# Kernel tuning notes

Measured on AMD Instinct MI355X. Metric: run time of the kernel, lower is better.

The kernel has to match this reference:

```python
import jax, jax.numpy as jnp
import numpy as np

B, N, C, H = 8192, 17, 512, 8
HD = C // H  # head dim = 64


def setup_inputs() -> dict:
    key = jax.random.key(0)
    ks = jax.random.split(key, 7)
    s = 0.02
    return {
        "x": jax.random.normal(ks[0], (B, N, C), dtype=jnp.float32),
        "W_qkv": jax.random.normal(ks[1], (C, 3 * C), dtype=jnp.float32) * s,
        "b_qkv": jax.random.normal(ks[2], (3 * C,), dtype=jnp.float32) * s,
        "outer": jax.random.normal(ks[3], (H, N, N), dtype=jnp.float32) * s,
        "alpha": jnp.ones((1,), dtype=jnp.float32),
        "W_proj": jax.random.normal(ks[4], (C, C), dtype=jnp.float32) * s,
        "b_proj": jax.random.normal(ks[5], (C,), dtype=jnp.float32) * s,
    }


def reference(x, W_qkv, b_qkv, outer, alpha, W_proj, b_proj):
    scale = HD ** -0.5
    qkv = x @ W_qkv + b_qkv                       # [B,N,3C]
    qkv = qkv.reshape(B, N, 3, H, HD)
    q = jnp.transpose(qkv[:, :, 0], (0, 2, 1, 3))  # [B,H,N,HD]
    k = jnp.transpose(qkv[:, :, 1], (0, 2, 1, 3))
    v = jnp.transpose(qkv[:, :, 2], (0, 2, 1, 3))
    # comb=False path: (q @ k^T + alpha * outer) * scale, softmax, @ v
    logits = (jnp.einsum('bhnd,bhmd->bhnm', q, k) + alpha * outer[None]) * scale
    attn = jax.nn.softmax(logits, axis=-1)        # [B,H,N,N]
    out = jnp.einsum('bhnm,bhmd->bhnd', attn, v)  # [B,H,N,HD]
    out = jnp.transpose(out, (0, 2, 1, 3)).reshape(B, N, C)
    return out @ W_proj + b_proj
```

## Files before the change

### kernel.cpp

```cpp
#include <hip/hip_runtime.h>
#include <stdint.h>


typedef __attribute__((ext_vector_type(4))) float f32x4;
typedef _Float16 f16x8 __attribute__((ext_vector_type(8)));
typedef _Float16 f16x4 __attribute__((ext_vector_type(4)));
typedef _Float16 f16x2 __attribute__((ext_vector_type(2)));

__device__ __forceinline__ unsigned short f2h(float f) {
  return __builtin_bit_cast(unsigned short, (_Float16)f);
}
__device__ __forceinline__ float h2f(unsigned short h) {
  return (float)__builtin_bit_cast(_Float16, h);
}
__device__ __forceinline__ float fdot2u(uint32_t a, uint32_t b, float c) {
  return __builtin_amdgcn_fdot2(__builtin_bit_cast(f16x2, a),
                                __builtin_bit_cast(f16x2, b), c, false);
}

#define GLOAD_LDS16(gptr, lptr)                                          \
  __builtin_amdgcn_global_load_lds(                                      \
      (__attribute__((address_space(1))) void*)(gptr),                   \
      (__attribute__((address_space(3))) void*)(lptr), 16, 0, 0)

#define VMCNT(n) asm volatile("s_waitcnt vmcnt(" #n ")" ::: "memory")

__device__ __forceinline__ f32x4 mfma16(f16x8 a, f16x8 b, f32x4 c) {
  return __builtin_amdgcn_mfma_f32_16x16x32_f16(a, b, c, 0, 0, 0);
}
__device__ __forceinline__ f32x4 mfma16k16(f16x4 a, f16x4 b, f32x4 c) {
  return __builtin_amdgcn_mfma_f32_16x16x16f16(a, b, c, 0, 0, 0);
}

__global__ __launch_bounds__(256) void k_cvt(const float* __restrict__ in,
                                             unsigned short* __restrict__ out,
                                             long n4) {
  long i = (long)blockIdx.x * 256 + threadIdx.x;
  if (i >= n4) return;
  float4 a = reinterpret_cast<const float4*>(in)[i];
  ushort4 o;
  o.x = f2h(a.x); o.y = f2h(a.y); o.z = f2h(a.z); o.w = f2h(a.w);
  reinterpret_cast<ushort4*>(out)[i] = o;
}

template <bool PERM>
__global__ __launch_bounds__(256) void k_cvt_t(const float* __restrict__ W,
                                               unsigned short* __restrict__ Wt,
                                               int K, int Norig) {
  int i = blockIdx.x * 256 + threadIdx.x;
  if (i >= K * Norig) return;
  int np = i / K, k = i - np * K;
  int n = np;
  if (PERM) {
    int h = np / 192, rem = np - h * 192;
    int t = rem >> 6, d = rem & 63;
    n = t * 512 + h * 64 + d;
  }
  Wt[i] = f2h(W[(size_t)k * Norig + n]);
}

__global__ __launch_bounds__(256) void k_permb(const float* __restrict__ b,
                                               float* __restrict__ bqp) {
  int np = blockIdx.x * 256 + threadIdx.x;
  if (np >= 1536) return;
  int h = np / 192, rem = np - h * 192;
  int t = rem >> 6, d = rem & 63;
  bqp[np] = b[t * 512 + h * 64 + d];
}

#define FBUFS 14336

__global__ __launch_bounds__(1024, 4) void k_fused(
    const unsigned short* __restrict__ A,
    const unsigned short* __restrict__ Bt,
    const float* __restrict__ bqp,
    const float* __restrict__ outer,
    const float* __restrict__ alpha_p,
    unsigned short* __restrict__ ao) {
  __shared__ __align__(16) unsigned short smem[64640];

  const int tid = threadIdx.x;
  const int w = tid >> 6, lane = tid & 63;
  const int wm = w >> 2, wn = w & 3;
  const int lr = lane & 15, lk = lane >> 4;

  const int g = (blockIdx.x & 7) * 547 + (blockIdx.x >> 3);
  const int mt = g >> 3, h = g & 7;
  const int batch0 = mt * 15;
  const int brow = batch0 * 17;
  const int bcol = h * 192;

  const int rsl = lane >> 2;
  const int swcol = ((lane & 3) ^ ((lane >> 3) & 3)) << 3;
  const bool cw2 = (w < 12);

  f32x4 acc[4][3];
#pragma unroll
  for (int m = 0; m < 4; m++)
#pragma unroll
    for (int n = 0; n < 3; n++) acc[m][n] = f32x4{0.f, 0.f, 0.f, 0.f};

  auto STAGE1 = [&](int t, int s) {
    unsigned short* dst = smem + (t & 3) * FBUFS + s * 512;
    const unsigned short* src;
    if (s < 16) {
      int gr = brow + s * 16 + rsl;
      if (gr > 139263) gr = 139263;
      src = A + (size_t)gr * 512 + t * 32 + swcol;
    } else {
      src = Bt + (size_t)(bcol + (s - 16) * 16 + rsl) * 512 + t * 32 + swcol;
    }
    GLOAD_LDS16(src, dst);
  };
  auto STAGE = [&](int t) {
    STAGE1(t, w);
    if (cw2) STAGE1(t, 16 + w);
  };

  STAGE(0); STAGE(1); STAGE(2);
  if (cw2) { VMCNT(4); } else { VMCNT(2); }
  __builtin_amdgcn_s_barrier();

  const int gx = (lk ^ ((lr >> 1) & 3)) << 3;
  for (int t = 0; t < 16; ++t) {
    if (t + 3 < 16) STAGE(t + 3);
    const unsigned short* bufp = smem + (t & 3) * FBUFS;
    const unsigned short* sa = bufp + (wm * 64 + lr) * 32 + gx;
    const unsigned short* sb = bufp + 8192 + (wn * 48 + lr) * 32 + gx;
    f16x8 a0 = *(const f16x8*)(sa);
    f16x8 a1 = *(const f16x8*)(sa + 512);
    f16x8 a2 = *(const f16x8*)(sa + 1024);
    f16x8 a3 = *(const f16x8*)(sa + 1536);
    f16x8 b0 = *(const f16x8*)(sb);
    f16x8 b1 = *(const f16x8*)(sb + 512);
    f16x8 b2 = *(const f16x8*)(sb + 1024);
    acc[0][0] = mfma16(a0, b0, acc[0][0]);
    acc[0][1] = mfma16(a0, b1, acc[0][1]);
    acc[0][2] = mfma16(a0, b2, acc[0][2]);
    acc[1][0] = mfma16(a1, b0, acc[1][0]);
    acc[1][1] = mfma16(a1, b1, acc[1][1]);
    acc[1][2] = mfma16(a1, b2, acc[1][2]);
    acc[2][0] = mfma16(a2, b0, acc[2][0]);
    acc[2][1] = mfma16(a2, b1, acc[2][1]);
    acc[2][2] = mfma16(a2, b2, acc[2][2]);
    acc[3][0] = mfma16(a3, b0, acc[3][0]);
    acc[3][1] = mfma16(a3, b1, acc[3][1]);
    acc[3][2] = mfma16(a3, b2, acc[3][2]);
    if (t < 13) {
      if (cw2) { VMCNT(4); } else { VMCNT(2); }
    } else if (t == 13) {
      if (cw2) { VMCNT(2); } else { VMCNT(1); }
    } else if (t == 14) {
      VMCNT(0);
    }
    __builtin_amdgcn_s_barrier();
  }

  unsigned short* SQ = smem;
  unsigned short* VT = smem + 34816;
  unsigned short* PL = smem + 57856;
  float* SE = (float*)(smem + 63616);

  {
    const int er0 = wm * 64 + (lane >> 4) * 4;
    const int ec0 = wn * 48 + lr;
#pragma unroll
    for (int nf = 0; nf < 3; ++nf) {
      const int col = ec0 + nf * 16;
      const float bv = bqp[bcol + col];
#pragma unroll
      for (int mf = 0; mf < 4; ++mf) {
        const int t0 = er0 + mf * 16;
        float v0 = acc[mf][nf][0] + bv, v1 = acc[mf][nf][1] + bv;
        float v2 = acc[mf][nf][2] + bv, v3 = acc[mf][nf][3] + bv;
        if (col < 128) {
          SQ[(t0 + 0) * 136 + col] = f2h(v0);
          SQ[(t0 + 1) * 136 + col] = f2h(v1);
          SQ[(t0 + 2) * 136 + col] = f2h(v2);
          SQ[(t0 + 3) * 136 + col] = f2h(v3);
        } else {
          const int d = col - 128;
#pragma unroll
          for (int rr = 0; rr < 4; ++rr) {
            const int tt = t0 + rr;
            const int bb = tt / 17, tl = tt - bb * 17;
            float vv = (rr == 0 ? v0 : rr == 1 ? v1 : rr == 2 ? v2 : v3);
            if (bb < 15) VT[bb * 1536 + d * 24 + tl] = f2h(vv);
          }
        }
      }
    }
  }
  __syncthreads();

  const int nb = min(15, 8192 - batch0);
  if (w < nb) {
    const float alpha = alpha_p[0];
    const int base = w * 17;
    unsigned short* PLw = PL + w * 384;
    unsigned short* VTw = VT + w * 1536;
    float* SEw = SE + w * 34;

    f32x4 sAcc = f32x4{0.f, 0.f, 0.f, 0.f};
#pragma unroll
    for (int kk = 0; kk < 2; ++kk) {
      f16x8 qa = *(const f16x8*)(SQ + (base + lr) * 136 + kk * 32 + lk * 8);
      f16x8 kb = *(const f16x8*)(SQ + (base + lr) * 136 + 64 + kk * 32 + lk * 8);
      sAcc = mfma16(qa, kb, sAcc);
    }

    if (lane < 33) {
      const int r_ = (lane < 16) ? lane : 16;
      const int m_ = (lane < 16) ? 16 : lane - 16;
      const uint4* qr = (const uint4*)(SQ + (base + r_) * 136);
      const uint4* kr = (const uint4*)(SQ + (base + m_) * 136 + 64);
      float dt = 0.f;
#pragma unroll
      for (int c = 0; c < 8; ++c) {
        uint4 qa = qr[c], ka = kr[c];
        dt = fdot2u(qa.x, ka.x, dt);
        dt = fdot2u(qa.y, ka.y, dt);
        dt = fdot2u(qa.z, ka.z, dt);
        dt = fdot2u(qa.w, ka.w, dt);
      }
      float sv = (dt + alpha * outer[h * 289 + r_ * 17 + m_]) * 0.125f;
      SEw[(lane < 16) ? lane : (17 + m_)] = sv;
    }
    __builtin_amdgcn_wave_barrier();
    asm volatile("" ::: "memory");

    const int g4 = (lane >> 4) * 4;
    float sp[4], rmax[4], p[4], pe[4], rsum[4], inv[4];
#pragma unroll
    for (int j = 0; j < 4; ++j) {
      sp[j] = (sAcc[j] + alpha * outer[h * 289 + (g4 + j) * 17 + lr]) * 0.125f;
      rmax[j] = sp[j];
    }
#pragma unroll
    for (int d = 1; d < 16; d <<= 1)
#pragma unroll
      for (int j = 0; j < 4; ++j)
        rmax[j] = fmaxf(rmax[j], __shfl_xor(rmax[j], d));
#pragma unroll
    for (int j = 0; j < 4; ++j) {
      float ec = SEw[g4 + j];
      rmax[j] = fmaxf(rmax[j], ec);
      p[j] = __expf(sp[j] - rmax[j]);
      pe[j] = __expf(ec - rmax[j]);
      rsum[j] = p[j];
    }
#pragma unroll
    for (int d = 1; d < 16; d <<= 1)
#pragma unroll
      for (int j = 0; j < 4; ++j) rsum[j] += __shfl_xor(rsum[j], d);
#pragma unroll
    for (int j = 0; j < 4; ++j) {
      rsum[j] += pe[j];
      inv[j] = 1.f / rsum[j];
      PLw[(g4 + j) * 24 + lr] = f2h(p[j]);
    }
    __builtin_amdgcn_wave_barrier();
    asm volatile("" ::: "memory");

    f16x4 pa = *(const f16x4*)(PLw + lr * 24 + lk * 4);
    f32x4 o[4];
    float v16[4];
#pragma unroll
    for (int nf = 0; nf < 4; ++nf) {
      f16x4 vb = *(const f16x4*)(VTw + (nf * 16 + lr) * 24 + lk * 4);
      o[nf] = mfma16k16(pa, vb, f32x4{0.f, 0.f, 0.f, 0.f});
      v16[nf] = h2f(VTw[(nf * 16 + lr) * 24 + 16]);
    }
    const size_t gr0 = (size_t)(brow + base) * 512 + h * 64;
#pragma unroll
    for (int nf = 0; nf < 4; ++nf)
#pragma unroll
      for (int j = 0; j < 4; ++j)
        ao[gr0 + (size_t)(g4 + j) * 512 + nf * 16 + lr] =
            f2h((o[nf][j] + pe[j] * v16[nf]) * inv[j]);

    {
      float mx16 = -1e30f;
#pragma unroll 1
      for (int m = 0; m < 17; ++m) mx16 = fmaxf(mx16, SEw[17 + m]);
      float o16 = 0.f, s16 = 0.f;
#pragma unroll 1
      for (int m = 0; m < 17; ++m) {
        float pm = __expf(SEw[17 + m] - mx16);
        s16 += pm;
        o16 += pm * h2f(VTw[lane * 24 + m]);
      }
      ao[gr0 + (size_t)16 * 512 + lane] = f2h(o16 / s16);
    }
  }
}

#define PBUFS 16384

__global__ __launch_bounds__(1024, 4) void k_proj(
    const unsigned short* __restrict__ A,
    const unsigned short* __restrict__ Bt,
    const float* __restrict__ bias,
    float* __restrict__ C) {
  __shared__ __align__(16) unsigned short smem[65536];

  const int tid = threadIdx.x;
  const int w = tid >> 6, lane = tid & 63;
  const int wm = w >> 2, wn = w & 3;
  const int lr = lane & 15, lk = lane >> 4;

  const int g = (blockIdx.x & 7) * 136 + (blockIdx.x >> 3);
  const int brow = (g >> 1) << 8;
  const int bcol = (g & 1) << 8;

  const int rsl = lane >> 2;
  const int swcol = ((lane & 3) ^ ((lane >> 3) & 3)) << 3;

  f32x4 acc[4][4];
#pragma unroll
  for (int m = 0; m < 4; m++)
#pragma unroll
    for (int n = 0; n < 4; n++) acc[m][n] = f32x4{0.f, 0.f, 0.f, 0.f};

  auto STAGE1 = [&](int t, int s) {
    unsigned short* dst = smem + (t & 3) * PBUFS + s * 512;
    const unsigned short* src =
        (s < 16) ? A + (size_t)(brow + s * 16 + rsl) * 512 + t * 32 + swcol
                 : Bt + (size_t)(bcol + (s - 16) * 16 + rsl) * 512 + t * 32 + swcol;
    GLOAD_LDS16(src, dst);
  };
  auto STAGE = [&](int t) {
    STAGE1(t, w);
    STAGE1(t, 16 + w);
  };

  STAGE(0); STAGE(1); STAGE(2);
  VMCNT(4);
  __builtin_amdgcn_s_barrier();

  const int gx = (lk ^ ((lr >> 1) & 3)) << 3;
  for (int t = 0; t < 16; ++t) {
    if (t + 3 < 16) STAGE(t + 3);
    const unsigned short* bufp = smem + (t & 3) * PBUFS;
    const unsigned short* sa = bufp + (wm * 64 + lr) * 32 + gx;
    const unsigned short* sb = bufp + 8192 + (wn * 64 + lr) * 32 + gx;
    f16x8 av[4], bv[4];
#pragma unroll
    for (int m = 0; m < 4; m++) av[m] = *(const f16x8*)(sa + m * 512);
#pragma unroll
    for (int n = 0; n < 4; n++) bv[n] = *(const f16x8*)(sb + n * 512);
#pragma unroll
    for (int m = 0; m < 4; m++)
#pragma unroll
      for (int n = 0; n < 4; n++)
        acc[m][n] = mfma16(av[m], bv[n], acc[m][n]);
    if (t < 13) {
      VMCNT(4);
    } else if (t == 13) {
      VMCNT(2);
    } else if (t == 14) {
      VMCNT(0);
    }
    __builtin_amdgcn_s_barrier();
  }

  const int orow = brow + wm * 64 + (lane >> 4) * 4;
  const int ocol0 = bcol + wn * 64 + lr;
#pragma unroll
  for (int n = 0; n < 4; n++) {
    const int col = ocol0 + n * 16;
    const float bv = bias[col];
#pragma unroll
    for (int m = 0; m < 4; m++) {
      const int row = orow + m * 16;
#pragma unroll
      for (int r = 0; r < 4; r++)
        C[(size_t)(row + r) * 512 + col] = acc[m][n][r] + bv;
    }
  }
}

extern "C" void kernel_launch(void* const* d_in, const int* in_sizes, int n_in,
                              void* d_out, int out_size, void* d_ws,
                              size_t ws_size, hipStream_t stream) {
  const float* x      = (const float*)d_in[0];
  const float* W_qkv  = (const float*)d_in[1];
  const float* b_qkv  = (const float*)d_in[2];
  const float* outer  = (const float*)d_in[3];
  const float* alpha  = (const float*)d_in[4];
  const float* W_proj = (const float*)d_in[5];
  const float* b_proj = (const float*)d_in[6];

  char* ws = (char*)d_ws;
  unsigned short* xb  = (unsigned short*)(ws);
  unsigned short* ao  = (unsigned short*)(ws + 142606336);
  unsigned short* wqt = (unsigned short*)(ws + 285212672);
  unsigned short* wpt = (unsigned short*)(ws + 286785536);
  float*          bqp = (float*)(ws + 287309824);

  k_cvt<<<dim3(69632), dim3(256), 0, stream>>>(x, xb, 17825792L);
  k_cvt_t<true><<<dim3(3072), dim3(256), 0, stream>>>(W_qkv, wqt, 512, 1536);
  k_cvt_t<false><<<dim3(1024), dim3(256), 0, stream>>>(W_proj, wpt, 512, 512);
  k_permb<<<dim3(6), dim3(256), 0, stream>>>(b_qkv, bqp);

  k_fused<<<dim3(4376), dim3(1024), 0, stream>>>(xb, wqt, bqp, outer, alpha, ao);

  k_proj<<<dim3(1088), dim3(1024), 0, stream>>>(ao, wpt, b_proj, (float*)d_out);
}
```

Before: 616.0 us.

## Fuse fp32-to-fp16 conversion of x into the fused QKV-attention kernel

Drops the separate x conversion kernel. The fused kernel now loads fp32 rows of x into registers, converts them to fp16 and writes them into swizzled LDS, while W_qkv tiles still arrive through direct global-to-LDS loads. To fit, the block shrinks from 1024 to 512 threads and from 15 to 7 batches per tile, with a smaller LDS footprint and a new grid size. This avoids writing and re-reading a half-precision copy of x. In exchange each head block reads the wider fp32 x directly, and converting through registers adds VALU work, LDS-wait stalls, and more redundant x traffic across the eight head blocks of each tile.

```diff
diff --git a/kernel.cpp b/kernel.cpp
--- a/kernel.cpp
+++ b/kernel.cpp
@@ -24,23 +24,13 @@
       (__attribute__((address_space(3))) void*)(lptr), 16, 0, 0)
 
 #define VMCNT(n) asm volatile("s_waitcnt vmcnt(" #n ")" ::: "memory")
+#define LGKM0 asm volatile("s_waitcnt lgkmcnt(0)" ::: "memory")
 
 __device__ __forceinline__ f32x4 mfma16(f16x8 a, f16x8 b, f32x4 c) {
   return __builtin_amdgcn_mfma_f32_16x16x32_f16(a, b, c, 0, 0, 0);
 }
 __device__ __forceinline__ f32x4 mfma16k16(f16x4 a, f16x4 b, f32x4 c) {
   return __builtin_amdgcn_mfma_f32_16x16x16f16(a, b, c, 0, 0, 0);
-}
-
-__global__ __launch_bounds__(256) void k_cvt(const float* __restrict__ in,
-                                             unsigned short* __restrict__ out,
-                                             long n4) {
-  long i = (long)blockIdx.x * 256 + threadIdx.x;
-  if (i >= n4) return;
-  float4 a = reinterpret_cast<const float4*>(in)[i];
-  ushort4 o;
-  o.x = f2h(a.x); o.y = f2h(a.y); o.z = f2h(a.z); o.w = f2h(a.w);
-  reinterpret_cast<ushort4*>(out)[i] = o;
 }
 
 template <bool PERM>
@@ -68,31 +58,73 @@
   bqp[np] = b[t * 512 + h * 64 + d];
 }
 
-#define FBUFS 14336
-
-__global__ __launch_bounds__(1024, 4) void k_fused(
-    const unsigned short* __restrict__ A,
+__global__ __launch_bounds__(512, 4) void k_fused(
+    const float* __restrict__ X,
     const unsigned short* __restrict__ Bt,
     const float* __restrict__ bqp,
     const float* __restrict__ outer,
     const float* __restrict__ alpha_p,
     unsigned short* __restrict__ ao) {
-  __shared__ __align__(16) unsigned short smem[64640];
+  __shared__ __align__(16) unsigned short smem[40960];
 
   const int tid = threadIdx.x;
   const int w = tid >> 6, lane = tid & 63;
   const int wm = w >> 2, wn = w & 3;
   const int lr = lane & 15, lk = lane >> 4;
 
-  const int g = (blockIdx.x & 7) * 547 + (blockIdx.x >> 3);
+  const int g = (blockIdx.x & 7) * 1171 + (blockIdx.x >> 3);
   const int mt = g >> 3, h = g & 7;
-  const int batch0 = mt * 15;
+  const int batch0 = mt * 7;
   const int brow = batch0 * 17;
   const int bcol = h * 192;
 
+  const bool cw2 = (w < 4);
+
+  const int r = lane >> 2;
+  const int g0 = (lane & 3) >> 1;
+  const int h0 = lane & 1;
+  const int sxr = (r >> 1) & 3;
+  const int cg0 = (((g0)     ^ sxr) << 1) | h0;
+  const int cg1 = (((g0 + 2) ^ sxr) << 1) | h0;
+  const int ld0 = g0 * 8 + h0 * 4;
+  const int ld1 = (g0 + 2) * 8 + h0 * 4;
+  int rowg = brow + w * 16 + r;
+  if (rowg > 139263) rowg = 139263;
+  const float* xrow = X + (size_t)rowg * 512;
+
+  f32x4 aA0, aA1, aB0, aB1;
+  auto A_LOAD0 = [&](int t) {
+    aA0 = *(const f32x4*)(xrow + t * 32 + cg0 * 4);
+    aA1 = *(const f32x4*)(xrow + t * 32 + cg1 * 4);
+  };
+  auto A_LOAD1 = [&](int t) {
+    aB0 = *(const f32x4*)(xrow + t * 32 + cg0 * 4);
+    aB1 = *(const f32x4*)(xrow + t * 32 + cg1 * 4);
+  };
+  auto A_WRITE = [&](int t, const f32x4& u0, const f32x4& u1) {
+    unsigned short* d = smem + (t & 3) * 10240 + w * 512 + r * 32;
+    ushort4 o0 = {f2h(u0[0]), f2h(u0[1]), f2h(u0[2]), f2h(u0[3])};
+    ushort4 o1 = {f2h(u1[0]), f2h(u1[1]), f2h(u1[2]), f2h(u1[3])};
+    *(ushort4*)(d + ld0) = o0;
+    *(ushort4*)(d + ld1) = o1;
+  };
   const int rsl = lane >> 2;
   const int swcol = ((lane & 3) ^ ((lane >> 3) & 3)) << 3;
-  const bool cw2 = (w < 12);
+  auto STAGE_B = [&](int t) {
+    {
+      unsigned short* dst = smem + (t & 3) * 10240 + 4096 + w * 512 + lane * 8;
+      const unsigned short* src =
+          Bt + (size_t)(bcol + w * 16 + rsl) * 512 + t * 32 + swcol;
+      GLOAD_LDS16(src, dst);
+    }
+    if (cw2) {
+      unsigned short* dst =
+          smem + (t & 3) * 10240 + 4096 + (8 + w) * 512 + lane * 8;
+      const unsigned short* src =
+          Bt + (size_t)(bcol + (8 + w) * 16 + rsl) * 512 + t * 32 + swcol;
+      GLOAD_LDS16(src, dst);
+    }
+  };
 
   f32x4 acc[4][3];
 #pragma unroll
@@ -100,33 +132,22 @@
 #pragma unroll
     for (int n = 0; n < 3; n++) acc[m][n] = f32x4{0.f, 0.f, 0.f, 0.f};
 
-  auto STAGE1 = [&](int t, int s) {
-    unsigned short* dst = smem + (t & 3) * FBUFS + s * 512;
-    const unsigned short* src;
-    if (s < 16) {
-      int gr = brow + s * 16 + rsl;
-      if (gr > 139263) gr = 139263;
-      src = A + (size_t)gr * 512 + t * 32 + swcol;
-    } else {
-      src = Bt + (size_t)(bcol + (s - 16) * 16 + rsl) * 512 + t * 32 + swcol;
-    }
-    GLOAD_LDS16(src, dst);
-  };
-  auto STAGE = [&](int t) {
-    STAGE1(t, w);
-    if (cw2) STAGE1(t, 16 + w);
-  };
-
-  STAGE(0); STAGE(1); STAGE(2);
-  if (cw2) { VMCNT(4); } else { VMCNT(2); }
+  A_LOAD0(0);
+  STAGE_B(0);
+  STAGE_B(1);
+  A_LOAD1(1);
+  STAGE_B(2);
+  if (cw2) { VMCNT(6); } else { VMCNT(4); }
+  A_WRITE(0, aA0, aA1);
+  LGKM0;
   __builtin_amdgcn_s_barrier();
 
   const int gx = (lk ^ ((lr >> 1) & 3)) << 3;
+#pragma unroll 2
   for (int t = 0; t < 16; ++t) {
-    if (t + 3 < 16) STAGE(t + 3);
-    const unsigned short* bufp = smem + (t & 3) * FBUFS;
+    const unsigned short* bufp = smem + (t & 3) * 10240;
     const unsigned short* sa = bufp + (wm * 64 + lr) * 32 + gx;
-    const unsigned short* sb = bufp + 8192 + (wn * 48 + lr) * 32 + gx;
+    const unsigned short* sb = bufp + 4096 + (wn * 48 + lr) * 32 + gx;
     f16x8 a0 = *(const f16x8*)(sa);
     f16x8 a1 = *(const f16x8*)(sa + 512);
     f16x8 a2 = *(const f16x8*)(sa + 1024);
@@ -146,20 +167,31 @@
     acc[3][0] = mfma16(a3, b0, acc[3][0]);
     acc[3][1] = mfma16(a3, b1, acc[3][1]);
     acc[3][2] = mfma16(a3, b2, acc[3][2]);
-    if (t < 13) {
-      if (cw2) { VMCNT(4); } else { VMCNT(2); }
+    if ((t & 1) == 0) {
+      if (t < 14) A_LOAD0(t + 2);
+    } else {
+      if (t < 14) A_LOAD1(t + 2);
+    }
+    if (t < 13) STAGE_B(t + 3);
+    if (t <= 12) {
+      if (cw2) { VMCNT(6); } else { VMCNT(4); }
     } else if (t == 13) {
-      if (cw2) { VMCNT(2); } else { VMCNT(1); }
+      if (cw2) { VMCNT(4); } else { VMCNT(3); }
     } else if (t == 14) {
       VMCNT(0);
     }
+    if (t < 15) {
+      if ((t & 1) == 0) A_WRITE(t + 1, aB0, aB1);
+      else              A_WRITE(t + 1, aA0, aA1);
+    }
+    LGKM0;
     __builtin_amdgcn_s_barrier();
   }
 
   unsigned short* SQ = smem;
-  unsigned short* VT = smem + 34816;
-  unsigned short* PL = smem + 57856;
-  float* SE = (float*)(smem + 63616);
+  unsigned short* VT = smem + 17408;
+  unsigned short* PL = smem + 29696;
+  float* SE = (float*)(smem + 32768);
 
   {
     const int er0 = wm * 64 + (lane >> 4) * 4;
@@ -185,7 +217,7 @@
             const int tt = t0 + rr;
             const int bb = tt / 17, tl = tt - bb * 17;
             float vv = (rr == 0 ? v0 : rr == 1 ? v1 : rr == 2 ? v2 : v3);
-            if (bb < 15) VT[bb * 1536 + d * 24 + tl] = f2h(vv);
+            if (bb < 7) VT[bb * 1536 + d * 24 + tl] = f2h(vv);
           }
         }
       }
@@ -193,7 +225,7 @@
   }
   __syncthreads();
 
-  const int nb = min(15, 8192 - batch0);
+  const int nb = min(7, 8192 - batch0);
   if (w < nb) {
     const float alpha = alpha_p[0];
     const int base = w * 17;
@@ -392,18 +424,16 @@
   const float* b_proj = (const float*)d_in[6];
 
   char* ws = (char*)d_ws;
-  unsigned short* xb  = (unsigned short*)(ws);
-  unsigned short* ao  = (unsigned short*)(ws + 142606336);
-  unsigned short* wqt = (unsigned short*)(ws + 285212672);
-  unsigned short* wpt = (unsigned short*)(ws + 286785536);
-  float*          bqp = (float*)(ws + 287309824);
-
-  k_cvt<<<dim3(69632), dim3(256), 0, stream>>>(x, xb, 17825792L);
+  unsigned short* ao  = (unsigned short*)(ws);
+  unsigned short* wqt = (unsigned short*)(ws + 142606336);
+  unsigned short* wpt = (unsigned short*)(ws + 144179200);
+  float*          bqp = (float*)(ws + 144703488);
+
   k_cvt_t<true><<<dim3(3072), dim3(256), 0, stream>>>(W_qkv, wqt, 512, 1536);
   k_cvt_t<false><<<dim3(1024), dim3(256), 0, stream>>>(W_proj, wpt, 512, 512);
   k_permb<<<dim3(6), dim3(256), 0, stream>>>(b_qkv, bqp);
 
-  k_fused<<<dim3(4376), dim3(1024), 0, stream>>>(xb, wqt, bqp, outer, alpha, ao);
+  k_fused<<<dim3(9368), dim3(512), 0, stream>>>(x, wqt, bqp, outer, alpha, ao);
 
   k_proj<<<dim3(1088), dim3(1024), 0, stream>>>(ao, wpt, b_proj, (float*)d_out);
 }
```

After: 668.6 us. 1.09x slower.

## Shrink fused QKV-attention block to 256 threads with larger per-wave tiles

Applied to the files above, without the earlier changes.

Reworks the fused QKV GEMM and attention kernel from 1024-thread blocks covering 15 batches to 256-thread blocks covering 7 batches. Each wave now computes a 64x96 tile (4x6 MFMA fragments) instead of 64x48, so each LDS fragment load feeds more MFMAs. Every wave stages 5 chunks per k-step, and the attention phase loops waves over batches. The intent is more register-level reuse and a smaller LDS footprint for better occupancy. In exchange it uses more accumulator registers and launches more blocks, and the 112-row M tile pads 119 rows up to 128, wasting more compute than before.

```diff
diff --git a/kernel.cpp b/kernel.cpp
--- a/kernel.cpp
+++ b/kernel.cpp
@@ -68,88 +68,76 @@
   bqp[np] = b[t * 512 + h * 64 + d];
 }
 
-#define FBUFS 14336
-
-__global__ __launch_bounds__(1024, 4) void k_fused(
+__global__ __launch_bounds__(256, 2) void k_fused(
     const unsigned short* __restrict__ A,
     const unsigned short* __restrict__ Bt,
     const float* __restrict__ bqp,
     const float* __restrict__ outer,
     const float* __restrict__ alpha_p,
     unsigned short* __restrict__ ao) {
-  __shared__ __align__(16) unsigned short smem[64640];
+  __shared__ __align__(16) unsigned short smem[40960];
 
   const int tid = threadIdx.x;
   const int w = tid >> 6, lane = tid & 63;
-  const int wm = w >> 2, wn = w & 3;
+  const int wm = w >> 1, wn = w & 1;
   const int lr = lane & 15, lk = lane >> 4;
 
-  const int g = (blockIdx.x & 7) * 547 + (blockIdx.x >> 3);
+  const int g = (blockIdx.x & 7) * 1171 + (blockIdx.x >> 3);
   const int mt = g >> 3, h = g & 7;
-  const int batch0 = mt * 15;
+  const int batch0 = mt * 7;
   const int brow = batch0 * 17;
   const int bcol = h * 192;
 
   const int rsl = lane >> 2;
   const int swcol = ((lane & 3) ^ ((lane >> 3) & 3)) << 3;
-  const bool cw2 = (w < 12);
-
-  f32x4 acc[4][3];
+
+  f32x4 acc[4][6];
 #pragma unroll
   for (int m = 0; m < 4; m++)
 #pragma unroll
-    for (int n = 0; n < 3; n++) acc[m][n] = f32x4{0.f, 0.f, 0.f, 0.f};
+    for (int n = 0; n < 6; n++) acc[m][n] = f32x4{0.f, 0.f, 0.f, 0.f};
 
   auto STAGE1 = [&](int t, int s) {
-    unsigned short* dst = smem + (t & 3) * FBUFS + s * 512;
+    unsigned short* dst = smem + (t & 3) * 10240 + s * 512;
     const unsigned short* src;
-    if (s < 16) {
+    if (s < 8) {
       int gr = brow + s * 16 + rsl;
       if (gr > 139263) gr = 139263;
       src = A + (size_t)gr * 512 + t * 32 + swcol;
     } else {
-      src = Bt + (size_t)(bcol + (s - 16) * 16 + rsl) * 512 + t * 32 + swcol;
+      src = Bt + (size_t)(bcol + (s - 8) * 16 + rsl) * 512 + t * 32 + swcol;
     }
     GLOAD_LDS16(src, dst);
   };
   auto STAGE = [&](int t) {
-    STAGE1(t, w);
-    if (cw2) STAGE1(t, 16 + w);
+#pragma unroll
+    for (int i = 0; i < 5; ++i) STAGE1(t, w * 5 + i);
   };
 
   STAGE(0); STAGE(1); STAGE(2);
-  if (cw2) { VMCNT(4); } else { VMCNT(2); }
+  VMCNT(10);
   __builtin_amdgcn_s_barrier();
 
   const int gx = (lk ^ ((lr >> 1) & 3)) << 3;
   for (int t = 0; t < 16; ++t) {
     if (t + 3 < 16) STAGE(t + 3);
-    const unsigned short* bufp = smem + (t & 3) * FBUFS;
+    const unsigned short* bufp = smem + (t & 3) * 10240;
     const unsigned short* sa = bufp + (wm * 64 + lr) * 32 + gx;
-    const unsigned short* sb = bufp + 8192 + (wn * 48 + lr) * 32 + gx;
-    f16x8 a0 = *(const f16x8*)(sa);
-    f16x8 a1 = *(const f16x8*)(sa + 512);
-    f16x8 a2 = *(const f16x8*)(sa + 1024);
-    f16x8 a3 = *(const f16x8*)(sa + 1536);
-    f16x8 b0 = *(const f16x8*)(sb);
-    f16x8 b1 = *(const f16x8*)(sb + 512);
-    f16x8 b2 = *(const f16x8*)(sb + 1024);
-    acc[0][0] = mfma16(a0, b0, acc[0][0]);
-    acc[0][1] = mfma16(a0, b1, acc[0][1]);
-    acc[0][2] = mfma16(a0, b2, acc[0][2]);
-    acc[1][0] = mfma16(a1, b0, acc[1][0]);
-    acc[1][1] = mfma16(a1, b1, acc[1][1]);
-    acc[1][2] = mfma16(a1, b2, acc[1][2]);
-    acc[2][0] = mfma16(a2, b0, acc[2][0]);
-    acc[2][1] = mfma16(a2, b1, acc[2][1]);
-    acc[2][2] = mfma16(a2, b2, acc[2][2]);
-    acc[3][0] = mfma16(a3, b0, acc[3][0]);
-    acc[3][1] = mfma16(a3, b1, acc[3][1]);
-    acc[3][2] = mfma16(a3, b2, acc[3][2]);
+    const unsigned short* sb = bufp + 4096 + (wn * 96 + lr) * 32 + gx;
+    f16x8 av[4], bv[6];
+#pragma unroll
+    for (int m = 0; m < 4; m++) av[m] = *(const f16x8*)(sa + m * 512);
+#pragma unroll
+    for (int n = 0; n < 6; n++) bv[n] = *(const f16x8*)(sb + n * 512);
+#pragma unroll
+    for (int m = 0; m < 4; m++)
+#pragma unroll
+      for (int n = 0; n < 6; n++)
+        acc[m][n] = mfma16(av[m], bv[n], acc[m][n]);
     if (t < 13) {
-      if (cw2) { VMCNT(4); } else { VMCNT(2); }
+      VMCNT(10);
     } else if (t == 13) {
-      if (cw2) { VMCNT(2); } else { VMCNT(1); }
+      VMCNT(5);
     } else if (t == 14) {
       VMCNT(0);
     }
@@ -157,22 +145,22 @@
   }
 
   unsigned short* SQ = smem;
-  unsigned short* VT = smem + 34816;
-  unsigned short* PL = smem + 57856;
-  float* SE = (float*)(smem + 63616);
+  unsigned short* VT = smem + 17408;
+  unsigned short* PL = smem + 29696;
+  float* SE = (float*)(smem + 32768);
 
   {
     const int er0 = wm * 64 + (lane >> 4) * 4;
-    const int ec0 = wn * 48 + lr;
-#pragma unroll
-    for (int nf = 0; nf < 3; ++nf) {
+    const int ec0 = wn * 96 + lr;
+#pragma unroll
+    for (int nf = 0; nf < 6; ++nf) {
       const int col = ec0 + nf * 16;
-      const float bv = bqp[bcol + col];
+      const float bv2 = bqp[bcol + col];
 #pragma unroll
       for (int mf = 0; mf < 4; ++mf) {
         const int t0 = er0 + mf * 16;
-        float v0 = acc[mf][nf][0] + bv, v1 = acc[mf][nf][1] + bv;
-        float v2 = acc[mf][nf][2] + bv, v3 = acc[mf][nf][3] + bv;
+        float v0 = acc[mf][nf][0] + bv2, v1 = acc[mf][nf][1] + bv2;
+        float v2 = acc[mf][nf][2] + bv2, v3 = acc[mf][nf][3] + bv2;
         if (col < 128) {
           SQ[(t0 + 0) * 136 + col] = f2h(v0);
           SQ[(t0 + 1) * 136 + col] = f2h(v1);
@@ -185,7 +173,7 @@
             const int tt = t0 + rr;
             const int bb = tt / 17, tl = tt - bb * 17;
             float vv = (rr == 0 ? v0 : rr == 1 ? v1 : rr == 2 ? v2 : v3);
-            if (bb < 15) VT[bb * 1536 + d * 24 + tl] = f2h(vv);
+            if (bb < 7) VT[bb * 1536 + d * 24 + tl] = f2h(vv);
           }
         }
       }
@@ -193,13 +181,13 @@
   }
   __syncthreads();
 
-  const int nb = min(15, 8192 - batch0);
-  if (w < nb) {
-    const float alpha = alpha_p[0];
-    const int base = w * 17;
-    unsigned short* PLw = PL + w * 384;
-    unsigned short* VTw = VT + w * 1536;
-    float* SEw = SE + w * 34;
+  const int nb = min(7, 8192 - batch0);
+  const float alpha = alpha_p[0];
+  for (int bb = w; bb < nb; bb += 4) {
+    const int base = bb * 17;
+    unsigned short* PLw = PL + bb * 384;
+    unsigned short* VTw = VT + bb * 1536;
+    float* SEw = SE + bb * 34;
 
     f32x4 sAcc = f32x4{0.f, 0.f, 0.f, 0.f};
 #pragma unroll
@@ -403,7 +391,7 @@
   k_cvt_t<false><<<dim3(1024), dim3(256), 0, stream>>>(W_proj, wpt, 512, 512);
   k_permb<<<dim3(6), dim3(256), 0, stream>>>(b_qkv, bqp);
 
-  k_fused<<<dim3(4376), dim3(1024), 0, stream>>>(xb, wqt, bqp, outer, alpha, ao);
+  k_fused<<<dim3(9368), dim3(256), 0, stream>>>(xb, wqt, bqp, outer, alpha, ao);
 
   k_proj<<<dim3(1088), dim3(1024), 0, stream>>>(ao, wpt, b_proj, (float*)d_out);
 }
```

Result: slower. 653.8 us (+6.1%).

## Halve fused block to 7 batches and load QKV weights straight into registers

Applied to the files above, without the earlier changes.

The fused QKV+attention kernel shrinks from 1024 to 512 threads per block, covering 7 batches (119 of 128 rows) per block instead of 15. The weight operand is no longer staged through LDS. Each wave now loads its B fragments from global memory into double-buffered registers, while only the A tile keeps using the LDS DMA ring. This cuts LDS use per block roughly in half to raise occupancy and reduce LDS traffic. The cost is more redundant global/L2 weight reads and more wasted padded rows per tile.

```diff
diff --git a/kernel.cpp b/kernel.cpp
--- a/kernel.cpp
+++ b/kernel.cpp
@@ -68,31 +68,28 @@
   bqp[np] = b[t * 512 + h * 64 + d];
 }
 
-#define FBUFS 14336
-
-__global__ __launch_bounds__(1024, 4) void k_fused(
+__global__ __launch_bounds__(512, 4) void k_fused(
     const unsigned short* __restrict__ A,
     const unsigned short* __restrict__ Bt,
     const float* __restrict__ bqp,
     const float* __restrict__ outer,
     const float* __restrict__ alpha_p,
     unsigned short* __restrict__ ao) {
-  __shared__ __align__(16) unsigned short smem[64640];
+  __shared__ __align__(16) unsigned short smem[33312];
 
   const int tid = threadIdx.x;
   const int w = tid >> 6, lane = tid & 63;
   const int wm = w >> 2, wn = w & 3;
   const int lr = lane & 15, lk = lane >> 4;
 
-  const int g = (blockIdx.x & 7) * 547 + (blockIdx.x >> 3);
+  const int g = (blockIdx.x & 7) * 1171 + (blockIdx.x >> 3);
   const int mt = g >> 3, h = g & 7;
-  const int batch0 = mt * 15;
+  const int batch0 = mt * 7;
   const int brow = batch0 * 17;
   const int bcol = h * 192;
 
   const int rsl = lane >> 2;
   const int swcol = ((lane & 3) ^ ((lane >> 3) & 3)) << 3;
-  const bool cw2 = (w < 12);
 
   f32x4 acc[4][3];
 #pragma unroll
@@ -100,66 +97,85 @@
 #pragma unroll
     for (int n = 0; n < 3; n++) acc[m][n] = f32x4{0.f, 0.f, 0.f, 0.f};
 
-  auto STAGE1 = [&](int t, int s) {
-    unsigned short* dst = smem + (t & 3) * FBUFS + s * 512;
-    const unsigned short* src;
-    if (s < 16) {
-      int gr = brow + s * 16 + rsl;
-      if (gr > 139263) gr = 139263;
-      src = A + (size_t)gr * 512 + t * 32 + swcol;
-    } else {
-      src = Bt + (size_t)(bcol + (s - 16) * 16 + rsl) * 512 + t * 32 + swcol;
-    }
-    GLOAD_LDS16(src, dst);
+  auto A_DMA = [&](int t) {
+    unsigned short* dst = smem + (t & 3) * 4096 + w * 512;
+    int gr = brow + w * 16 + rsl;
+    if (gr > 139263) gr = 139263;
+    GLOAD_LDS16(A + (size_t)gr * 512 + t * 32 + swcol, dst);
   };
-  auto STAGE = [&](int t) {
-    STAGE1(t, w);
-    if (cw2) STAGE1(t, 16 + w);
+
+  const unsigned short* bp =
+      Bt + (size_t)(bcol + wn * 48 + lr) * 512 + lk * 8;
+  f16x8 bvA[3], bvB[3];
+  auto B_LOAD_A = [&](int t) {
+#pragma unroll
+    for (int nf = 0; nf < 3; ++nf)
+      bvA[nf] = *(const f16x8*)(bp + t * 32 + nf * 8192);
   };
-
-  STAGE(0); STAGE(1); STAGE(2);
-  if (cw2) { VMCNT(4); } else { VMCNT(2); }
+  auto B_LOAD_B = [&](int t) {
+#pragma unroll
+    for (int nf = 0; nf < 3; ++nf)
+      bvB[nf] = *(const f16x8*)(bp + t * 32 + nf * 8192);
+  };
+
+  A_DMA(0);
+  B_LOAD_A(0);
+  A_DMA(1);
+  VMCNT(4);
   __builtin_amdgcn_s_barrier();
 
   const int gx = (lk ^ ((lr >> 1) & 3)) << 3;
+#pragma unroll 2
   for (int t = 0; t < 16; ++t) {
-    if (t + 3 < 16) STAGE(t + 3);
-    const unsigned short* bufp = smem + (t & 3) * FBUFS;
-    const unsigned short* sa = bufp + (wm * 64 + lr) * 32 + gx;
-    const unsigned short* sb = bufp + 8192 + (wn * 48 + lr) * 32 + gx;
+    const unsigned short* sa = smem + (t & 3) * 4096 + (wm * 64 + lr) * 32 + gx;
     f16x8 a0 = *(const f16x8*)(sa);
     f16x8 a1 = *(const f16x8*)(sa + 512);
     f16x8 a2 = *(const f16x8*)(sa + 1024);
     f16x8 a3 = *(const f16x8*)(sa + 1536);
-    f16x8 b0 = *(const f16x8*)(sb);
-    f16x8 b1 = *(const f16x8*)(sb + 512);
-    f16x8 b2 = *(const f16x8*)(sb + 1024);
-    acc[0][0] = mfma16(a0, b0, acc[0][0]);
-    acc[0][1] = mfma16(a0, b1, acc[0][1]);
-    acc[0][2] = mfma16(a0, b2, acc[0][2]);
-    acc[1][0] = mfma16(a1, b0, acc[1][0]);
-    acc[1][1] = mfma16(a1, b1, acc[1][1]);
-    acc[1][2] = mfma16(a1, b2, acc[1][2]);
-    acc[2][0] = mfma16(a2, b0, acc[2][0]);
-    acc[2][1] = mfma16(a2, b1, acc[2][1]);
-    acc[2][2] = mfma16(a2, b2, acc[2][2]);
-    acc[3][0] = mfma16(a3, b0, acc[3][0]);
-    acc[3][1] = mfma16(a3, b1, acc[3][1]);
-    acc[3][2] = mfma16(a3, b2, acc[3][2]);
-    if (t < 13) {
-      if (cw2) { VMCNT(4); } else { VMCNT(2); }
-    } else if (t == 13) {
-      if (cw2) { VMCNT(2); } else { VMCNT(1); }
+    if ((t & 1) == 0) {
+      acc[0][0] = mfma16(a0, bvA[0], acc[0][0]);
+      acc[0][1] = mfma16(a0, bvA[1], acc[0][1]);
+      acc[0][2] = mfma16(a0, bvA[2], acc[0][2]);
+      acc[1][0] = mfma16(a1, bvA[0], acc[1][0]);
+      acc[1][1] = mfma16(a1, bvA[1], acc[1][1]);
+      acc[1][2] = mfma16(a1, bvA[2], acc[1][2]);
+      acc[2][0] = mfma16(a2, bvA[0], acc[2][0]);
+      acc[2][1] = mfma16(a2, bvA[1], acc[2][1]);
+      acc[2][2] = mfma16(a2, bvA[2], acc[2][2]);
+      acc[3][0] = mfma16(a3, bvA[0], acc[3][0]);
+      acc[3][1] = mfma16(a3, bvA[1], acc[3][1]);
+      acc[3][2] = mfma16(a3, bvA[2], acc[3][2]);
+      if (t + 1 < 16) B_LOAD_B(t + 1);
+    } else {
+      acc[0][0] = mfma16(a0, bvB[0], acc[0][0]);
+      acc[0][1] = mfma16(a0, bvB[1], acc[0][1]);
+      acc[0][2] = mfma16(a0, bvB[2], acc[0][2]);
+      acc[1][0] = mfma16(a1, bvB[0], acc[1][0]);
+      acc[1][1] = mfma16(a1, bvB[1], acc[1][1]);
+      acc[1][2] = mfma16(a1, bvB[2], acc[1][2]);
+      acc[2][0] = mfma16(a2, bvB[0], acc[2][0]);
+      acc[2][1] = mfma16(a2, bvB[1], acc[2][1]);
+      acc[2][2] = mfma16(a2, bvB[2], acc[2][2]);
+      acc[3][0] = mfma16(a3, bvB[0], acc[3][0]);
+      acc[3][1] = mfma16(a3, bvB[1], acc[3][1]);
+      acc[3][2] = mfma16(a3, bvB[2], acc[3][2]);
+      if (t + 1 < 16) B_LOAD_A(t + 1);
+    }
+    if (t + 2 < 16) A_DMA(t + 2);
+    if (t <= 13) {
+      VMCNT(4);
     } else if (t == 14) {
+      VMCNT(3);
+    } else {
       VMCNT(0);
     }
     __builtin_amdgcn_s_barrier();
   }
 
   unsigned short* SQ = smem;
-  unsigned short* VT = smem + 34816;
-  unsigned short* PL = smem + 57856;
-  float* SE = (float*)(smem + 63616);
+  unsigned short* VT = smem + 17408;
+  unsigned short* PL = smem + 29696;
+  float* SE = (float*)(smem + 32768);
 
   {
     const int er0 = wm * 64 + (lane >> 4) * 4;
@@ -185,7 +201,7 @@
             const int tt = t0 + rr;
             const int bb = tt / 17, tl = tt - bb * 17;
             float vv = (rr == 0 ? v0 : rr == 1 ? v1 : rr == 2 ? v2 : v3);
-            if (bb < 15) VT[bb * 1536 + d * 24 + tl] = f2h(vv);
+            if (bb < 7) VT[bb * 1536 + d * 24 + tl] = f2h(vv);
           }
         }
       }
@@ -193,7 +209,7 @@
   }
   __syncthreads();
 
-  const int nb = min(15, 8192 - batch0);
+  const int nb = min(7, 8192 - batch0);
   if (w < nb) {
     const float alpha = alpha_p[0];
     const int base = w * 17;
@@ -403,7 +419,7 @@
   k_cvt_t<false><<<dim3(1024), dim3(256), 0, stream>>>(W_proj, wpt, 512, 512);
   k_permb<<<dim3(6), dim3(256), 0, stream>>>(b_qkv, bqp);
 
-  k_fused<<<dim3(4376), dim3(1024), 0, stream>>>(xb, wqt, bqp, outer, alpha, ao);
+  k_fused<<<dim3(9368), dim3(512), 0, stream>>>(xb, wqt, bqp, outer, alpha, ao);
 
   k_proj<<<dim3(1088), dim3(1024), 0, stream>>>(ao, wpt, b_proj, (float*)d_out);
 }
```

New measurement: 725.8 us. +17.8%, slower.
